# Kernel optimization log

Measured on AMD Instinct MI355X. Metric: run time of the kernel, lower is better.

## Reference

```python
import jax, jax.numpy as jnp
import numpy as np

N = 32768      # total nodes
E = 524288     # edges (avg degree 16)
HID = 256      # hidden_dim
H = 8          # heads
C = HID // H   # head dim = 32
G = 64         # graphs in batch
NPG = N // G   # nodes per graph = 512
EDIM = 2       # edge feature dim
NEG_SLOPE = 0.2  # PyG GATv2 default


def setup_inputs():
    key = jax.random.key(0)
    ks = jax.random.split(key, 12)
    s = 0.05
    return dict(
        x=jax.random.normal(ks[0], (N, HID), jnp.float32),
        edge_attr=jax.random.normal(ks[1], (E, EDIM), jnp.float32),
        # GATv2Conv params
        W_l=jax.random.normal(ks[2], (HID, HID), jnp.float32) * s,
        b_l=jnp.zeros((HID,), jnp.float32),
        W_r=jax.random.normal(ks[3], (HID, HID), jnp.float32) * s,
        b_r=jnp.zeros((HID,), jnp.float32),
        W_e=jax.random.normal(ks[4], (EDIM, HID), jnp.float32) * s,
        att=jax.random.normal(ks[5], (H, C), jnp.float32) * s,
        bias_gat=jnp.zeros((HID,), jnp.float32),
        # MultiheadAttention params (torch packed qkv layout)
        in_proj_w=jax.random.normal(ks[6], (3 * HID, HID), jnp.float32) * s,
        in_proj_b=jnp.zeros((3 * HID,), jnp.float32),
        out_proj_w=jax.random.normal(ks[7], (HID, HID), jnp.float32) * s,
        out_proj_b=jnp.zeros((HID,), jnp.float32),
        alpha_param=jnp.array(0.5, jnp.float32),
        # FFN
        W1=jax.random.normal(ks[8], (HID, 4 * HID), jnp.float32) * s,
        b1=jnp.zeros((4 * HID,), jnp.float32),
        W2=jax.random.normal(ks[9], (4 * HID, HID), jnp.float32) * s,
        b2=jnp.zeros((HID,), jnp.float32),
        # LayerNorms
        g1=jnp.ones((HID,), jnp.float32), be1=jnp.zeros((HID,), jnp.float32),
        g2=jnp.ones((HID,), jnp.float32), be2=jnp.zeros((HID,), jnp.float32),
        g3=jnp.ones((HID,), jnp.float32), be3=jnp.zeros((HID,), jnp.float32),
        edge_index=jax.random.randint(ks[10], (2, E), 0, N, jnp.int32),
        batch=jnp.repeat(jnp.arange(G, dtype=jnp.int32), NPG),
    )


def _ln(x, g, b, eps=1e-5):
    m = jnp.mean(x, -1, keepdims=True)
    v = jnp.mean((x - m) ** 2, -1, keepdims=True)
    return (x - m) * jax.lax.rsqrt(v + eps) * g + b


def _gatv2(x, edge_index, edge_attr, W_l, b_l, W_r, b_r, W_e, att, bias_gat):
    src, dst = edge_index[0], edge_index[1]
    # PyG add_self_loops with fill_value='mean': self-loop edge_attr at node i
    # is the mean of edge_attr over edges incoming to i (0 if none).
    deg = jax.ops.segment_sum(jnp.ones((E,), x.dtype), dst, num_segments=N)
    ea_mean = jax.ops.segment_sum(edge_attr, dst, num_segments=N) / jnp.maximum(deg, 1.0)[:, None]
    loop = jnp.arange(N, dtype=src.dtype)
    src2 = jnp.concatenate([src, loop])
    dst2 = jnp.concatenate([dst, loop])
    ea2 = jnp.concatenate([edge_attr, ea_mean], axis=0)  # [E+N, 2]
    xl = (x @ W_l + b_l).reshape(N, H, C)  # source transform (messages)
    xr = (x @ W_r + b_r).reshape(N, H, C)  # target transform
    ee = (ea2 @ W_e).reshape(-1, H, C)
    e = jax.nn.leaky_relu(xl[src2] + xr[dst2] + ee, NEG_SLOPE)  # [E+N, H, C]
    score = jnp.einsum('ehc,hc->eh', e, att)  # [E+N, H]
    # scatter softmax over incoming edges of each target node
    smax = jax.lax.stop_gradient(jax.ops.segment_max(score, dst2, num_segments=N))
    ex = jnp.exp(score - smax[dst2])
    ssum = jax.ops.segment_sum(ex, dst2, num_segments=N)
    alpha = ex / ssum[dst2]  # [E+N, H]
    out = jax.ops.segment_sum(alpha[:, :, None] * xl[src2], dst2, num_segments=N)
    return out.reshape(N, HID) + bias_gat


def _mha(xg, in_proj_w, in_proj_b, out_proj_w, out_proj_b):
    # xg: [G, NPG, HID]; torch nn.MultiheadAttention (batch_first, eval mode)
    qkv = xg @ in_proj_w.T + in_proj_b
    q, k, v = jnp.split(qkv, 3, axis=-1)
    q = q.reshape(G, NPG, H, C)
    k = k.reshape(G, NPG, H, C)
    v = v.reshape(G, NPG, H, C)
    scores = jnp.einsum('gqhd,gkhd->ghqk', q, k) / jnp.sqrt(jnp.float32(C))
    p = jax.nn.softmax(scores, axis=-1)
    o = jnp.einsum('ghqk,gkhd->gqhd', p, v).reshape(G, NPG, HID)
    return o @ out_proj_w.T + out_proj_b


def reference(x, edge_attr, W_l, b_l, W_r, b_r, W_e, att, bias_gat,
              in_proj_w, in_proj_b, out_proj_w, out_proj_b, alpha_param,
              W1, b1, W2, b2, g1, be1, g2, be2, g3, be3, edge_index, batch):
    local_out = _ln(
        _gatv2(x, edge_index, edge_attr, W_l, b_l, W_r, b_r, W_e, att, bias_gat),
        g1, be1)
    # batch is sorted with equal-sized graphs -> the per-graph ragged
    # attention loop equals one batched [G, NPG, NPG] attention
    xg = x.reshape(G, NPG, HID)
    global_out = _mha(xg, in_proj_w, in_proj_b, out_proj_w, out_proj_b).reshape(N, HID)
    global_out = _ln(global_out, g2, be2)
    a = jax.nn.sigmoid(alpha_param)
    combined = a * local_out + (1.0 - a) * global_out
    ffn = jax.nn.gelu(combined @ W1 + b1, approximate=False) @ W2 + b2
    return _ln(combined + ffn, g3, be3)
```

## Files before the change

kernel.cpp:

```cpp
#include <hip/hip_runtime.h>
#include <math.h>

#define N_NODES 32768
#define E_EDGES 524288
#define HIDDEN  256
#define NPG     512
#define NGRAPH  64
#define NHEAD   8
#define CDIM    32

typedef unsigned short bf16;
typedef __attribute__((ext_vector_type(8))) short short8;
typedef __attribute__((ext_vector_type(4))) float f4;

#define AS1 __attribute__((address_space(1)))
#define AS3 __attribute__((address_space(3)))

__device__ __forceinline__ void cp16(const bf16* g, bf16* l) {
    __builtin_amdgcn_global_load_lds((AS1 const unsigned int*)(const void*)g,
                                     (AS3 unsigned int*)(void*)l, 16, 0, 0);
}

__device__ inline float bf2f(unsigned short u) {
    union { unsigned int i; float f; } v; v.i = ((unsigned int)u) << 16; return v.f;
}
__device__ inline unsigned short f2bf(float f) {
    union { float f; unsigned int i; } v; v.f = f;
    unsigned int x = v.i;
    return (unsigned short)((x + 0x7FFFu + ((x >> 16) & 1u)) >> 16);
}
__device__ inline float4 load4(const float* p) { return *(const float4*)p; }
__device__ inline float4 load4(const bf16* p) {
    ushort4 u = *(const ushort4*)p;
    return make_float4(bf2f(u.x), bf2f(u.y), bf2f(u.z), bf2f(u.w));
}
__device__ inline void store4(float* p, float4 v) { *(float4*)p = v; }
__device__ inline void store4(bf16* p, float4 v) {
    ushort4 u; u.x = f2bf(v.x); u.y = f2bf(v.y); u.z = f2bf(v.z); u.w = f2bf(v.w);
    *(ushort4*)p = u;
}


__global__ void zero_kernel(float* deg, float* ea_sum, int* fill) {
    int i = blockIdx.x * blockDim.x + threadIdx.x;
    if (i < 2 * N_NODES) ea_sum[i] = 0.0f;
    if (i < N_NODES) { deg[i] = 0.0f; fill[i] = 0; }
}

__global__ void deg_kernel(const int* __restrict__ ei, const float* __restrict__ edge_attr,
                           float* deg, float* ea_sum) {
    int e = blockIdx.x * blockDim.x + threadIdx.x;
    if (e >= E_EDGES) return;
    int d = ei[E_EDGES + e];
    atomicAdd(&deg[d], 1.0f);
    atomicAdd(&ea_sum[2 * d + 0], edge_attr[2 * e + 0]);
    atomicAdd(&ea_sum[2 * d + 1], edge_attr[2 * e + 1]);
}

__global__ void eamean_kernel(const float* __restrict__ deg, float* ea_mean) {
    int i = blockIdx.x * blockDim.x + threadIdx.x;
    if (i >= N_NODES) return;
    float dm = fmaxf(deg[i], 1.0f);
    ea_mean[2 * i + 0] /= dm;
    ea_mean[2 * i + 1] /= dm;
}

__global__ __launch_bounds__(1024) void scan_kernel(const float* __restrict__ deg, int* row_ptr) {
    __shared__ int part[1024];
    int t = threadIdx.x;
    int base = t * 32;
    int loc[32];
    int s = 0;
    #pragma unroll
    for (int j = 0; j < 32; j++) {
        loc[j] = s;
        s += (int)deg[base + j] + 1;
    }
    int mysum = s;
    part[t] = s;
    __syncthreads();
    for (int off = 1; off < 1024; off <<= 1) {
        int v = 0;
        if (t >= off) v = part[t - off];
        __syncthreads();
        part[t] += v;
        __syncthreads();
    }
    int offset = part[t] - mysum;
    #pragma unroll
    for (int j = 0; j < 32; j++) row_ptr[base + j] = offset + loc[j];
    if (t == 1023) row_ptr[N_NODES] = part[1023];
}

__global__ void fill_kernel(const int* __restrict__ ei, const int* __restrict__ row_ptr,
                            int* fill, int* col) {
    int tid = blockIdx.x * blockDim.x + threadIdx.x;
    if (tid >= E_EDGES + N_NODES) return;
    int d;
    if (tid < E_EDGES) d = ei[E_EDGES + tid];
    else               d = tid - E_EDGES;
    int pos = row_ptr[d] + atomicAdd(&fill[d], 1);
    col[pos] = tid;
}

__global__ void convall(const float* __restrict__ x,
                        const float* __restrict__ W_l, const float* __restrict__ W_r,
                        const float* __restrict__ W1, const float* __restrict__ W2,
                        const float* __restrict__ in_proj_w, const float* __restrict__ out_proj_w,
                        const float* __restrict__ b_l, const float* __restrict__ b_r,
                        bf16* xb, bf16* wlrb, bf16* w1b, bf16* w2b,
                        bf16* wipb, bf16* wopb, float* blr)
{
    int b = blockIdx.x, t = threadIdx.x;
    if (b < 8192) {
        int i = b * 256 + t;
        store4(&xb[i * 4], *(const float4*)&x[i * 4]);
    } else if (b < 8448) {
        int i = (b - 8192) * 256 + t; int k = i >> 8, n = i & 255;
        wlrb[n * 256 + k] = f2bf(W_l[i]);
    } else if (b < 8704) {
        int i = (b - 8448) * 256 + t; int k = i >> 8, n = i & 255;
        wlrb[(256 + n) * 256 + k] = f2bf(W_r[i]);
    } else if (b < 9728) {
        int i = (b - 8704) * 256 + t; int k = i >> 10, n = i & 1023;
        w1b[n * 256 + k] = f2bf(W1[i]);
    } else if (b < 10752) {
        int i = (b - 9728) * 256 + t; int k = i >> 8, n = i & 255;
        w2b[n * 1024 + k] = f2bf(W2[i]);
    } else if (b < 10944) {
        int i = (b - 10752) * 256 + t;
        store4(&wipb[i * 4], *(const float4*)&in_proj_w[i * 4]);
    } else if (b < 11008) {
        int i = (b - 10944) * 256 + t;
        store4(&wopb[i * 4], *(const float4*)&out_proj_w[i * 4]);
    } else {
        blr[t] = b_l[t]; blr[256 + t] = b_r[t];
    }
}

template <int EPI>
__global__ __launch_bounds__(256) void mfma_gemm(
    const bf16* __restrict__ A, const bf16* __restrict__ Wb,
    const float* __restrict__ bias, const bf16* __restrict__ res,
    bf16* __restrict__ C, int M, int N, int K)
{
    __shared__ bf16 lds[2 * 128 * 64];
    bf16* As = lds;
    bf16* Bs = lds + 128 * 64;
    int tid = threadIdx.x;
    int wave = tid >> 6, lane = tid & 63;
    int quad = lane >> 4, l16 = lane & 15;
    int n0 = blockIdx.x * 128, m0 = blockIdx.y * 128;
    int wm = (wave & 1) * 64, wn = (wave >> 1) * 64;

    f4 acc[4][4] = {};

    int srow = tid >> 3;
    int scol = (tid & 7) * 8;

    for (int k0 = 0; k0 < K; k0 += 64) {
        #pragma unroll
        for (int i = 0; i < 4; i++) {
            int row = i * 32 + srow;
            cp16(&A[(size_t)(m0 + row) * K + k0 + scol], &As[row * 64 + scol]);
            cp16(&Wb[(size_t)(n0 + row) * K + k0 + scol], &Bs[row * 64 + scol]);
        }
        __syncthreads();
        #pragma unroll
        for (int ks = 0; ks < 2; ks++) {
            short8 af[4], bfr[4];
            #pragma unroll
            for (int mt = 0; mt < 4; mt++)
                af[mt] = *(const short8*)&As[(wm + mt * 16 + l16) * 64 + ks * 32 + quad * 8];
            #pragma unroll
            for (int nt = 0; nt < 4; nt++)
                bfr[nt] = *(const short8*)&Bs[(wn + nt * 16 + l16) * 64 + ks * 32 + quad * 8];
            #pragma unroll
            for (int mt = 0; mt < 4; mt++)
                #pragma unroll
                for (int nt = 0; nt < 4; nt++)
                    acc[mt][nt] = __builtin_amdgcn_mfma_f32_16x16x32_bf16(
                        af[mt], bfr[nt], acc[mt][nt], 0, 0, 0);
        }
        __syncthreads();
    }

    float* epi = (float*)lds + wave * 16 * 68;
    int row = lane >> 2;
    int cb = (lane & 3) * 16;
    int gn = n0 + wn + cb;
    float bb[16];
    *(float4*)&bb[0]  = *(const float4*)&bias[gn + 0];
    *(float4*)&bb[4]  = *(const float4*)&bias[gn + 4];
    *(float4*)&bb[8]  = *(const float4*)&bias[gn + 8];
    *(float4*)&bb[12] = *(const float4*)&bias[gn + 12];

    for (int mt = 0; mt < 4; mt++) {
        #pragma unroll
        for (int nt = 0; nt < 4; nt++)
            #pragma unroll
            for (int r = 0; r < 4; r++)
                epi[(quad * 4 + r) * 68 + nt * 16 + l16] = acc[mt][nt][r];
        float vv[16];
        *(float4*)&vv[0]  = *(float4*)&epi[row * 68 + cb + 0];
        *(float4*)&vv[4]  = *(float4*)&epi[row * 68 + cb + 4];
        *(float4*)&vv[8]  = *(float4*)&epi[row * 68 + cb + 8];
        *(float4*)&vv[12] = *(float4*)&epi[row * 68 + cb + 12];
        int gm = m0 + wm + mt * 16 + row;
        #pragma unroll
        for (int j = 0; j < 16; j++) vv[j] += bb[j];
        if (EPI == 1) {
            #pragma unroll
            for (int j = 0; j < 16; j++)
                vv[j] = 0.5f * vv[j] * (1.0f + erff(vv[j] * 0.70710678118654752f));
        } else if (EPI == 2) {
            ushort rr[16];
            const bf16* rp = &res[(size_t)gm * N + gn];
            *(int4*)&rr[0] = *(const int4*)&rp[0];
            *(int4*)&rr[8] = *(const int4*)&rp[8];
            #pragma unroll
            for (int j = 0; j < 16; j++) vv[j] += bf2f(rr[j]);
        }
        ushort o16[16];
        #pragma unroll
        for (int j = 0; j < 16; j++) o16[j] = f2bf(vv[j]);
        bf16* cp;
        if (EPI == 3) {
            bf16* dst = (gn < 256) ? C : (bf16*)res;
            int goff = (gn < 256) ? gn : gn - 256;
            cp = &dst[(size_t)gm * 256 + goff];
        } else {
            cp = &C[(size_t)gm * N + gn];
        }
        *(int4*)&cp[0] = *(int4*)&o16[0];
        *(int4*)&cp[8] = *(int4*)&o16[8];
    }
}

__global__ __launch_bounds__(256) void attn_mfma(
    const bf16* __restrict__ qkv, bf16* __restrict__ attnout)
{
    __shared__ bf16 Ks[128 * 40];
    __shared__ bf16 Vs[128 * 40];
    __shared__ bf16 Pb[4 * 64 * 40];
    __shared__ float lsumS[4][64];

    int b = blockIdx.x;
    int g = b >> 4, h = (b >> 1) & 7, hlf = b & 1;
    int tid = threadIdx.x;
    int wave = tid >> 6, lane = tid & 63;
    int quad = lane >> 4, l16 = lane & 15;
    int qbase = hlf * 256 + wave * 64;
    bf16* Pw = &Pb[wave * 64 * 40];
    const float SCALE = 0.17677669529663687f;

    short8 qf[4];
    #pragma unroll
    for (int qt = 0; qt < 4; qt++) {
        size_t node = (size_t)(g * NPG + qbase + qt * 16 + l16);
        qf[qt] = *(const short8*)&qkv[node * 768 + h * CDIM + quad * 8];
    }

    f4 oacc[4][2] = {};
    float ls[4] = {0.f, 0.f, 0.f, 0.f};

    for (int c = 0; c < 4; c++) {
        int kk0 = c * 128;
        __syncthreads();
        #pragma unroll
        for (int i = 0; i < 2; i++) {
            int idx = i * 256 + tid;
            int key = idx >> 2, kc = (idx & 3) * 8;
            const bf16* bp = &qkv[(size_t)(g * NPG + kk0 + key) * 768 + h * CDIM + kc];
            *(int4*)&Ks[key * 40 + kc] = *(const int4*)(bp + 256);
            *(int4*)&Vs[key * 40 + kc] = *(const int4*)(bp + 512);
        }
        __syncthreads();

        for (int sub = 0; sub < 4; sub++) {
            int ks0 = sub * 32;
            short8 kf[2];
            #pragma unroll
            for (int kt = 0; kt < 2; kt++)
                kf[kt] = *(const short8*)&Ks[(ks0 + kt * 16 + l16) * 40 + quad * 8];
            #pragma unroll
            for (int kt = 0; kt < 2; kt++) {
                #pragma unroll
                for (int qt = 0; qt < 4; qt++) {
                    f4 z = {0.f, 0.f, 0.f, 0.f};
                    f4 st = __builtin_amdgcn_mfma_f32_16x16x32_bf16(kf[kt], qf[qt], z, 0, 0, 0);
                    ushort pk[4];
                    float s4 = 0.f;
                    #pragma unroll
                    for (int r = 0; r < 4; r++) {
                        float p = __expf(st[r] * SCALE);
                        s4 += p;
                        pk[r] = f2bf(p);
                    }
                    ls[qt] += s4;
                    *(uint2*)&Pw[(qt * 16 + l16) * 40 + kt * 16 + quad * 4] = *(uint2*)pk;
                }
            }
            short8 vf[2];
            #pragma unroll
            for (int dt = 0; dt < 2; dt++) {
                ushort vtmp[8];
                #pragma unroll
                for (int j = 0; j < 8; j++)
                    vtmp[j] = Vs[(ks0 + quad * 8 + j) * 40 + dt * 16 + l16];
                vf[dt] = *(short8*)vtmp;
            }
            #pragma unroll
            for (int mt = 0; mt < 4; mt++) {
                short8 pf = *(const short8*)&Pw[(mt * 16 + l16) * 40 + quad * 8];
                #pragma unroll
                for (int dt = 0; dt < 2; dt++)
                    oacc[mt][dt] = __builtin_amdgcn_mfma_f32_16x16x32_bf16(
                        pf, vf[dt], oacc[mt][dt], 0, 0, 0);
            }
        }
    }

    #pragma unroll
    for (int qt = 0; qt < 4; qt++) {
        float l = ls[qt];
        l += __shfl_xor(l, 16);
        l += __shfl_xor(l, 32);
        if (quad == 0) lsumS[wave][qt * 16 + l16] = l;
    }
    __builtin_amdgcn_s_waitcnt(0);

    #pragma unroll
    for (int mt = 0; mt < 4; mt++) {
        #pragma unroll
        for (int dt = 0; dt < 2; dt++) {
            #pragma unroll
            for (int r = 0; r < 4; r++) {
                float denom = lsumS[wave][mt * 16 + quad * 4 + r];
                float v = oacc[mt][dt][r] / denom;
                size_t node = (size_t)(g * NPG + qbase + mt * 16 + quad * 4 + r);
                attnout[node * HIDDEN + h * CDIM + dt * 16 + l16] = f2bf(v);
            }
        }
    }
}

__device__ __forceinline__ void fetchmeta(
    int i, int re, int node, const int* __restrict__ col, const int* __restrict__ ei,
    const float* __restrict__ edge_attr, const float* __restrict__ ea_mean,
    int& s, float& a0, float& a1)
{
    if (i < re) {
        int e = col[i];
        if (e < E_EDGES) {
            s = ei[e]; a0 = edge_attr[2 * e]; a1 = edge_attr[2 * e + 1];
        } else {
            s = node; a0 = ea_mean[2 * node]; a1 = ea_mean[2 * node + 1];
        }
    } else {
        s = node; a0 = 0.f; a1 = 0.f;
    }
}

__global__ __launch_bounds__(256) void gat_kernel(
    const bf16* __restrict__ xl, const bf16* __restrict__ xr,
    const int* __restrict__ row_ptr, const int* __restrict__ col,
    const int* __restrict__ ei, const float* __restrict__ edge_attr,
    const float* __restrict__ ea_mean,
    const float* __restrict__ W_e, const float* __restrict__ att,
    const float* __restrict__ bias_gat,
    const float* __restrict__ g1, const float* __restrict__ be1,
    bf16* __restrict__ out)
{
    __shared__ float pacc[2][260];
    __shared__ float plsum[2][64];
    int wave = threadIdx.x >> 6;
    int lane = threadIdx.x & 63;
    int nloc = wave >> 1, half = wave & 1;
    int node = blockIdx.x * 2 + nloc;
    int cb = lane * 4;

    float4 xr4 = load4(&xr[(size_t)node * 256 + cb]);
    float4 we0 = *(const float4*)&W_e[cb];
    float4 we1 = *(const float4*)&W_e[HIDDEN + cb];
    float4 at4 = *(const float4*)&att[cb];

    int rs = row_ptr[node], re = row_ptr[node + 1];

    float lsum = 0.f;
    float acc0 = 0.f, acc1 = 0.f, acc2 = 0.f, acc3 = 0.f;

    int i0 = rs + half;
    int s0, s1; float a00, a01, a10, a11;
    fetchmeta(i0,     re, node, col, ei, edge_attr, ea_mean, s0, a00, a01);
    fetchmeta(i0 + 2, re, node, col, ei, edge_attr, ea_mean, s1, a10, a11);
    ushort4 xu0 = *(const ushort4*)&xl[(size_t)s0 * 256 + cb];

    for (int i = i0; i < re; i += 2) {
        int s2; float a20, a21;
        fetchmeta(i + 4, re, node, col, ei, edge_attr, ea_mean, s2, a20, a21);
        ushort4 xu1 = *(const ushort4*)&xl[(size_t)s1 * 256 + cb];

        float4 xl4 = make_float4(bf2f(xu0.x), bf2f(xu0.y), bf2f(xu0.z), bf2f(xu0.w));
        float t, p = 0.f;
        t = xl4.x + xr4.x + a00 * we0.x + a01 * we1.x; t = (t > 0.f) ? t : 0.2f * t; p += t * at4.x;
        t = xl4.y + xr4.y + a00 * we0.y + a01 * we1.y; t = (t > 0.f) ? t : 0.2f * t; p += t * at4.y;
        t = xl4.z + xr4.z + a00 * we0.z + a01 * we1.z; t = (t > 0.f) ? t : 0.2f * t; p += t * at4.z;
        t = xl4.w + xr4.w + a00 * we0.w + a01 * we1.w; t = (t > 0.f) ? t : 0.2f * t; p += t * at4.w;
        p += __shfl_xor(p, 1);
        p += __shfl_xor(p, 2);
        p += __shfl_xor(p, 4);
        float w = __expf(p);
        lsum += w;
        acc0 += w * xl4.x; acc1 += w * xl4.y; acc2 += w * xl4.z; acc3 += w * xl4.w;

        s0 = s1; a00 = a10; a01 = a11; xu0 = xu1;
        s1 = s2; a10 = a20; a11 = a21;
    }

    if (half) {
        plsum[nloc][lane] = lsum;
        pacc[nloc][cb + 0] = acc0; pacc[nloc][cb + 1] = acc1;
        pacc[nloc][cb + 2] = acc2; pacc[nloc][cb + 3] = acc3;
    }
    __syncthreads();
    if (!half) {
        lsum += plsum[nloc][lane];
        acc0 += pacc[nloc][cb + 0]; acc1 += pacc[nloc][cb + 1];
        acc2 += pacc[nloc][cb + 2]; acc3 += pacc[nloc][cb + 3];

        float inv = 1.0f / lsum;
        float v0 = acc0 * inv + bias_gat[cb + 0];
        float v1 = acc1 * inv + bias_gat[cb + 1];
        float v2 = acc2 * inv + bias_gat[cb + 2];
        float v3 = acc3 * inv + bias_gat[cb + 3];

        float s = v0 + v1 + v2 + v3;
        #pragma unroll
        for (int m = 1; m < 64; m <<= 1) s += __shfl_xor(s, m);
        float mean = s * (1.0f / 256.0f);
        float d0 = v0 - mean, d1 = v1 - mean, d2 = v2 - mean, d3 = v3 - mean;
        float sq = d0 * d0 + d1 * d1 + d2 * d2 + d3 * d3;
        #pragma unroll
        for (int m = 1; m < 64; m <<= 1) sq += __shfl_xor(sq, m);
        float rstd = rsqrtf(sq * (1.0f / 256.0f) + 1e-5f);
        float4 o;
        o.x = d0 * rstd * g1[cb + 0] + be1[cb + 0];
        o.y = d1 * rstd * g1[cb + 1] + be1[cb + 1];
        o.z = d2 * rstd * g1[cb + 2] + be1[cb + 2];
        o.w = d3 * rstd * g1[cb + 3] + be1[cb + 3];
        store4(&out[(size_t)node * HIDDEN + cb], o);
    }
}

__global__ __launch_bounds__(256) void combine_kernel(
    const bf16* __restrict__ gout, const bf16* __restrict__ localout,
    const float* __restrict__ alpha_p,
    const float* __restrict__ g2, const float* __restrict__ be2,
    bf16* __restrict__ combined)
{
    int wave = threadIdx.x >> 6;
    int lane = threadIdx.x & 63;
    int node = blockIdx.x * 4 + wave;
    int cb = lane * 4;
    float4 gv = load4(&gout[(size_t)node * HIDDEN + cb]);
    float s = gv.x + gv.y + gv.z + gv.w;
    #pragma unroll
    for (int m = 1; m < 64; m <<= 1) s += __shfl_xor(s, m);
    float mean = s * (1.0f / 256.0f);
    float d0 = gv.x - mean, d1 = gv.y - mean, d2 = gv.z - mean, d3 = gv.w - mean;
    float sq = d0 * d0 + d1 * d1 + d2 * d2 + d3 * d3;
    #pragma unroll
    for (int m = 1; m < 64; m <<= 1) sq += __shfl_xor(sq, m);
    float rstd = rsqrtf(sq * (1.0f / 256.0f) + 1e-5f);
    float n0 = d0 * rstd * g2[cb + 0] + be2[cb + 0];
    float n1 = d1 * rstd * g2[cb + 1] + be2[cb + 1];
    float n2 = d2 * rstd * g2[cb + 2] + be2[cb + 2];
    float n3 = d3 * rstd * g2[cb + 3] + be2[cb + 3];
    float a = 1.0f / (1.0f + __expf(-alpha_p[0]));
    float4 lv = load4(&localout[(size_t)node * HIDDEN + cb]);
    float4 o;
    o.x = a * lv.x + (1.0f - a) * n0;
    o.y = a * lv.y + (1.0f - a) * n1;
    o.z = a * lv.z + (1.0f - a) * n2;
    o.w = a * lv.w + (1.0f - a) * n3;
    store4(&combined[(size_t)node * HIDDEN + cb], o);
}

__global__ __launch_bounds__(256) void finalln_kernel(
    const bf16* __restrict__ ffn,
    const float* __restrict__ g3, const float* __restrict__ be3,
    float* __restrict__ out)
{
    int wave = threadIdx.x >> 6;
    int lane = threadIdx.x & 63;
    int node = blockIdx.x * 4 + wave;
    int cb = lane * 4;
    float4 v = load4(&ffn[(size_t)node * HIDDEN + cb]);
    float s = v.x + v.y + v.z + v.w;
    #pragma unroll
    for (int m = 1; m < 64; m <<= 1) s += __shfl_xor(s, m);
    float mean = s * (1.0f / 256.0f);
    float d0 = v.x - mean, d1 = v.y - mean, d2 = v.z - mean, d3 = v.w - mean;
    float sq = d0 * d0 + d1 * d1 + d2 * d2 + d3 * d3;
    #pragma unroll
    for (int m = 1; m < 64; m <<= 1) sq += __shfl_xor(sq, m);
    float rstd = rsqrtf(sq * (1.0f / 256.0f) + 1e-5f);
    float4 o;
    o.x = d0 * rstd * g3[cb + 0] + be3[cb + 0];
    o.y = d1 * rstd * g3[cb + 1] + be3[cb + 1];
    o.z = d2 * rstd * g3[cb + 2] + be3[cb + 2];
    o.w = d3 * rstd * g3[cb + 3] + be3[cb + 3];
    *(float4*)&out[(size_t)node * HIDDEN + cb] = o;
}

extern "C" void kernel_launch(void* const* d_in, const int* in_sizes, int n_in,
                              void* d_out, int out_size, void* d_ws, size_t ws_size,
                              hipStream_t stream) {
    const float* x          = (const float*)d_in[0];
    const float* edge_attr  = (const float*)d_in[1];
    const float* W_l        = (const float*)d_in[2];
    const float* b_l        = (const float*)d_in[3];
    const float* W_r        = (const float*)d_in[4];
    const float* b_r        = (const float*)d_in[5];
    const float* W_e        = (const float*)d_in[6];
    const float* att        = (const float*)d_in[7];
    const float* bias_gat   = (const float*)d_in[8];
    const float* in_proj_w  = (const float*)d_in[9];
    const float* in_proj_b  = (const float*)d_in[10];
    const float* out_proj_w = (const float*)d_in[11];
    const float* out_proj_b = (const float*)d_in[12];
    const float* alpha_p    = (const float*)d_in[13];
    const float* W1         = (const float*)d_in[14];
    const float* b1         = (const float*)d_in[15];
    const float* W2         = (const float*)d_in[16];
    const float* b2         = (const float*)d_in[17];
    const float* g1  = (const float*)d_in[18];
    const float* be1 = (const float*)d_in[19];
    const float* g2  = (const float*)d_in[20];
    const float* be2 = (const float*)d_in[21];
    const float* g3  = (const float*)d_in[22];
    const float* be3 = (const float*)d_in[23];
    const int* edge_index = (const int*)d_in[24];

    char* base = (char*)d_ws;
    const size_t MB = 1024 * 1024;
    const size_t KB = 1024;
    float* deg     = (float*)(base + 0);
    float* ea_mean = (float*)(base + 131072);
    int*   fill    = (int*)  (base + 393216);
    int*   row_ptr = (int*)  (base + 524288);
    int*   col     = (int*)  (base + 786432);
    bf16* wlrb = (bf16*)(base + 3 * MB);
    bf16* wipb = (bf16*)(base + 3 * MB + 256 * KB);
    bf16* wopb = (bf16*)(base + 3 * MB + 640 * KB);
    bf16* w1b  = (bf16*)(base + 3 * MB + 768 * KB);
    bf16* w2b  = (bf16*)(base + 3 * MB + 1280 * KB);
    float* blr = (float*)(base + 5 * MB);
    bf16* xb       = (bf16*)(base + 8 * MB);
    bf16* qkv      = (bf16*)(base + 24 * MB);
    bf16* attnout  = (bf16*)(base + 72 * MB);
    bf16* gout     = (bf16*)(base + 24 * MB);
    bf16* xl       = (bf16*)(base + 40 * MB);
    bf16* xr       = (bf16*)(base + 56 * MB);
    bf16* localout = (bf16*)(base + 72 * MB);
    bf16* combined = (bf16*)(base + 8 * MB);
    bf16* h1h      = (bf16*)(base + 24 * MB);
    bf16* ffn      = (bf16*)(base + 56 * MB);
    float* out = (float*)d_out;

    zero_kernel<<<(2 * N_NODES + 255) / 256, 256, 0, stream>>>(deg, ea_mean, fill);
    deg_kernel<<<E_EDGES / 256, 256, 0, stream>>>(edge_index, edge_attr, deg, ea_mean);
    eamean_kernel<<<N_NODES / 256, 256, 0, stream>>>(deg, ea_mean);
    scan_kernel<<<1, 1024, 0, stream>>>(deg, row_ptr);
    fill_kernel<<<(E_EDGES + N_NODES) / 256, 256, 0, stream>>>(edge_index, row_ptr, fill, col);

    convall<<<11009, 256, 0, stream>>>(x, W_l, W_r, W1, W2, in_proj_w, out_proj_w,
                                       b_l, b_r, xb, wlrb, w1b, w2b, wipb, wopb, blr);

    mfma_gemm<0><<<dim3(6, 256), 256, 0, stream>>>(
        xb, wipb, in_proj_b, (const bf16*)nullptr, qkv, N_NODES, 768, 256);
    attn_mfma<<<NGRAPH * NHEAD * 2, 256, 0, stream>>>(qkv, attnout);
    mfma_gemm<0><<<dim3(2, 256), 256, 0, stream>>>(
        attnout, wopb, out_proj_b, (const bf16*)nullptr, gout, N_NODES, 256, 256);

    mfma_gemm<3><<<dim3(4, 256), 256, 0, stream>>>(
        xb, wlrb, blr, (const bf16*)xr, xl, N_NODES, 512, 256);
    gat_kernel<<<N_NODES / 2, 256, 0, stream>>>(
        xl, xr, row_ptr, col, edge_index, edge_attr, ea_mean,
        W_e, att, bias_gat, g1, be1, localout);

    combine_kernel<<<N_NODES / 4, 256, 0, stream>>>(
        gout, localout, alpha_p, g2, be2, combined);

    for (int hh = 0; hh < 2; hh++) {
        const bf16* ch = combined + (size_t)hh * 16384 * 256;
        bf16* fh = ffn + (size_t)hh * 16384 * 256;
        mfma_gemm<1><<<dim3(8, 128), 256, 0, stream>>>(
            ch, w1b, b1, (const bf16*)nullptr, h1h, 16384, 1024, 256);
        mfma_gemm<2><<<dim3(2, 128), 256, 0, stream>>>(
            h1h, w2b, b2, ch, fh, 16384, 256, 1024);
    }

    finalln_kernel<<<N_NODES / 4, 256, 0, stream>>>(ffn, g3, be3, out);
}
```

Before: 616.3 us.

## Transpose V in LDS for attention and restructure GAT gather to one wave per node

The attention kernel now stores V transposed in shared memory, so each lane reads its MFMA B-operand as one 16-byte vector instead of eight strided scalar LDS reads. The GAT kernel drops the two-waves-per-node split and its LDS reduction. Each wave now handles one node and processes four edges per iteration, with four row gathers issued together and the next four edges' metadata prefetched. The gather change aims to raise memory-level parallelism and remove a block barrier, at the cost of more registers and wasted masked lanes on the tail of each edge list.

After: 664.7 us. +7.9%, slower.

```diff
diff --git a/kernel.cpp b/kernel.cpp
--- a/kernel.cpp
+++ b/kernel.cpp
@@ -241,7 +241,7 @@
     const bf16* __restrict__ qkv, bf16* __restrict__ attnout)
 {
     __shared__ bf16 Ks[128 * 40];
-    __shared__ bf16 Vs[128 * 40];
+    __shared__ bf16 Vt[32 * 136];
     __shared__ bf16 Pb[4 * 64 * 40];
     __shared__ float lsumS[4][64];
 
@@ -271,9 +271,17 @@
         for (int i = 0; i < 2; i++) {
             int idx = i * 256 + tid;
             int key = idx >> 2, kc = (idx & 3) * 8;
-            const bf16* bp = &qkv[(size_t)(g * NPG + kk0 + key) * 768 + h * CDIM + kc];
-            *(int4*)&Ks[key * 40 + kc] = *(const int4*)(bp + 256);
-            *(int4*)&Vs[key * 40 + kc] = *(const int4*)(bp + 512);
+            *(int4*)&Ks[key * 40 + kc] =
+                *(const int4*)&qkv[(size_t)(g * NPG + kk0 + key) * 768 + 256 + h * CDIM + kc];
+        }
+        {
+            int key = tid >> 1, dblk = (tid & 1) * 16;
+            ushort tmp[16];
+            const bf16* vp = &qkv[(size_t)(g * NPG + kk0 + key) * 768 + 512 + h * CDIM + dblk];
+            *(int4*)&tmp[0] = *(const int4*)&vp[0];
+            *(int4*)&tmp[8] = *(const int4*)&vp[8];
+            #pragma unroll
+            for (int j = 0; j < 16; j++) Vt[(dblk + j) * 136 + key] = tmp[j];
         }
         __syncthreads();
 
@@ -303,13 +311,8 @@
             }
             short8 vf[2];
             #pragma unroll
-            for (int dt = 0; dt < 2; dt++) {
-                ushort vtmp[8];
-                #pragma unroll
-                for (int j = 0; j < 8; j++)
-                    vtmp[j] = Vs[(ks0 + quad * 8 + j) * 40 + dt * 16 + l16];
-                vf[dt] = *(short8*)vtmp;
-            }
+            for (int dt = 0; dt < 2; dt++)
+                vf[dt] = *(const short8*)&Vt[(dt * 16 + l16) * 136 + ks0 + quad * 8];
             #pragma unroll
             for (int mt = 0; mt < 4; mt++) {
                 short8 pf = *(const short8*)&Pw[(mt * 16 + l16) * 40 + quad * 8];
@@ -342,23 +345,6 @@
                 attnout[node * HIDDEN + h * CDIM + dt * 16 + l16] = f2bf(v);
             }
         }
-    }
-}
-
-__device__ __forceinline__ void fetchmeta(
-    int i, int re, int node, const int* __restrict__ col, const int* __restrict__ ei,
-    const float* __restrict__ edge_attr, const float* __restrict__ ea_mean,
-    int& s, float& a0, float& a1)
-{
-    if (i < re) {
-        int e = col[i];
-        if (e < E_EDGES) {
-            s = ei[e]; a0 = edge_attr[2 * e]; a1 = edge_attr[2 * e + 1];
-        } else {
-            s = node; a0 = ea_mean[2 * node]; a1 = ea_mean[2 * node + 1];
-        }
-    } else {
-        s = node; a0 = 0.f; a1 = 0.f;
     }
 }
 
@@ -372,12 +358,9 @@
     const float* __restrict__ g1, const float* __restrict__ be1,
     bf16* __restrict__ out)
 {
-    __shared__ float pacc[2][260];
-    __shared__ float plsum[2][64];
     int wave = threadIdx.x >> 6;
     int lane = threadIdx.x & 63;
-    int nloc = wave >> 1, half = wave & 1;
-    int node = blockIdx.x * 2 + nloc;
+    int node = blockIdx.x * 4 + wave;
     int cb = lane * 4;
 
     float4 xr4 = load4(&xr[(size_t)node * 256 + cb]);
@@ -390,67 +373,75 @@
     float lsum = 0.f;
     float acc0 = 0.f, acc1 = 0.f, acc2 = 0.f, acc3 = 0.f;
 
-    int i0 = rs + half;
-    int s0, s1; float a00, a01, a10, a11;
-    fetchmeta(i0,     re, node, col, ei, edge_attr, ea_mean, s0, a00, a01);
-    fetchmeta(i0 + 2, re, node, col, ei, edge_attr, ea_mean, s1, a10, a11);
-    ushort4 xu0 = *(const ushort4*)&xl[(size_t)s0 * 256 + cb];
-
-    for (int i = i0; i < re; i += 2) {
-        int s2; float a20, a21;
-        fetchmeta(i + 4, re, node, col, ei, edge_attr, ea_mean, s2, a20, a21);
-        ushort4 xu1 = *(const ushort4*)&xl[(size_t)s1 * 256 + cb];
-
-        float4 xl4 = make_float4(bf2f(xu0.x), bf2f(xu0.y), bf2f(xu0.z), bf2f(xu0.w));
-        float t, p = 0.f;
-        t = xl4.x + xr4.x + a00 * we0.x + a01 * we1.x; t = (t > 0.f) ? t : 0.2f * t; p += t * at4.x;
-        t = xl4.y + xr4.y + a00 * we0.y + a01 * we1.y; t = (t > 0.f) ? t : 0.2f * t; p += t * at4.y;
-        t = xl4.z + xr4.z + a00 * we0.z + a01 * we1.z; t = (t > 0.f) ? t : 0.2f * t; p += t * at4.z;
-        t = xl4.w + xr4.w + a00 * we0.w + a01 * we1.w; t = (t > 0.f) ? t : 0.2f * t; p += t * at4.w;
-        p += __shfl_xor(p, 1);
-        p += __shfl_xor(p, 2);
-        p += __shfl_xor(p, 4);
-        float w = __expf(p);
-        lsum += w;
-        acc0 += w * xl4.x; acc1 += w * xl4.y; acc2 += w * xl4.z; acc3 += w * xl4.w;
-
-        s0 = s1; a00 = a10; a01 = a11; xu0 = xu1;
-        s1 = s2; a10 = a20; a11 = a21;
-    }
-
-    if (half) {
-        plsum[nloc][lane] = lsum;
-        pacc[nloc][cb + 0] = acc0; pacc[nloc][cb + 1] = acc1;
-        pacc[nloc][cb + 2] = acc2; pacc[nloc][cb + 3] = acc3;
-    }
-    __syncthreads();
-    if (!half) {
-        lsum += plsum[nloc][lane];
-        acc0 += pacc[nloc][cb + 0]; acc1 += pacc[nloc][cb + 1];
-        acc2 += pacc[nloc][cb + 2]; acc3 += pacc[nloc][cb + 3];
-
-        float inv = 1.0f / lsum;
-        float v0 = acc0 * inv + bias_gat[cb + 0];
-        float v1 = acc1 * inv + bias_gat[cb + 1];
-        float v2 = acc2 * inv + bias_gat[cb + 2];
-        float v3 = acc3 * inv + bias_gat[cb + 3];
-
-        float s = v0 + v1 + v2 + v3;
-        #pragma unroll
-        for (int m = 1; m < 64; m <<= 1) s += __shfl_xor(s, m);
-        float mean = s * (1.0f / 256.0f);
-        float d0 = v0 - mean, d1 = v1 - mean, d2 = v2 - mean, d3 = v3 - mean;
-        float sq = d0 * d0 + d1 * d1 + d2 * d2 + d3 * d3;
-        #pragma unroll
-        for (int m = 1; m < 64; m <<= 1) sq += __shfl_xor(sq, m);
-        float rstd = rsqrtf(sq * (1.0f / 256.0f) + 1e-5f);
-        float4 o;
-        o.x = d0 * rstd * g1[cb + 0] + be1[cb + 0];
-        o.y = d1 * rstd * g1[cb + 1] + be1[cb + 1];
-        o.z = d2 * rstd * g1[cb + 2] + be1[cb + 2];
-        o.w = d3 * rstd * g1[cb + 3] + be1[cb + 3];
-        store4(&out[(size_t)node * HIDDEN + cb], o);
-    }
+    int s[4]; float ax[4], ay[4];
+    #pragma unroll
+    for (int j = 0; j < 4; j++) {
+        int idx = rs + j;
+        if (idx < re) {
+            int e = col[idx];
+            if (e < E_EDGES) { s[j] = ei[e]; ax[j] = edge_attr[2 * e]; ay[j] = edge_attr[2 * e + 1]; }
+            else { s[j] = node; ax[j] = ea_mean[2 * node]; ay[j] = ea_mean[2 * node + 1]; }
+        } else { s[j] = node; ax[j] = 0.f; ay[j] = 0.f; }
+    }
+
+    for (int i = rs; i < re; i += 4) {
+        ushort4 xu[4];
+        #pragma unroll
+        for (int j = 0; j < 4; j++)
+            xu[j] = *(const ushort4*)&xl[(size_t)s[j] * 256 + cb];
+
+        int sn[4]; float axn[4], ayn[4];
+        int in0 = i + 4;
+        #pragma unroll
+        for (int j = 0; j < 4; j++) {
+            int idx = in0 + j;
+            if (idx < re) {
+                int e = col[idx];
+                if (e < E_EDGES) { sn[j] = ei[e]; axn[j] = edge_attr[2 * e]; ayn[j] = edge_attr[2 * e + 1]; }
+                else { sn[j] = node; axn[j] = ea_mean[2 * node]; ayn[j] = ea_mean[2 * node + 1]; }
+            } else { sn[j] = node; axn[j] = 0.f; ayn[j] = 0.f; }
+        }
+
+        #pragma unroll
+        for (int j = 0; j < 4; j++) {
+            float4 x4 = make_float4(bf2f(xu[j].x), bf2f(xu[j].y), bf2f(xu[j].z), bf2f(xu[j].w));
+            float t, p = 0.f;
+            t = x4.x + xr4.x + ax[j] * we0.x + ay[j] * we1.x; t = (t > 0.f) ? t : 0.2f * t; p += t * at4.x;
+            t = x4.y + xr4.y + ax[j] * we0.y + ay[j] * we1.y; t = (t > 0.f) ? t : 0.2f * t; p += t * at4.y;
+            t = x4.z + xr4.z + ax[j] * we0.z + ay[j] * we1.z; t = (t > 0.f) ? t : 0.2f * t; p += t * at4.z;
+            t = x4.w + xr4.w + ax[j] * we0.w + ay[j] * we1.w; t = (t > 0.f) ? t : 0.2f * t; p += t * at4.w;
+            p += __shfl_xor(p, 1);
+            p += __shfl_xor(p, 2);
+            p += __shfl_xor(p, 4);
+            float w = (i + j < re) ? __expf(p) : 0.f;
+            lsum += w;
+            acc0 += w * x4.x; acc1 += w * x4.y; acc2 += w * x4.z; acc3 += w * x4.w;
+        }
+        #pragma unroll
+        for (int j = 0; j < 4; j++) { s[j] = sn[j]; ax[j] = axn[j]; ay[j] = ayn[j]; }
+    }
+
+    float inv = 1.0f / lsum;
+    float v0 = acc0 * inv + bias_gat[cb + 0];
+    float v1 = acc1 * inv + bias_gat[cb + 1];
+    float v2 = acc2 * inv + bias_gat[cb + 2];
+    float v3 = acc3 * inv + bias_gat[cb + 3];
+
+    float sm = v0 + v1 + v2 + v3;
+    #pragma unroll
+    for (int m = 1; m < 64; m <<= 1) sm += __shfl_xor(sm, m);
+    float mean = sm * (1.0f / 256.0f);
+    float d0 = v0 - mean, d1 = v1 - mean, d2 = v2 - mean, d3 = v3 - mean;
+    float sq = d0 * d0 + d1 * d1 + d2 * d2 + d3 * d3;
+    #pragma unroll
+    for (int m = 1; m < 64; m <<= 1) sq += __shfl_xor(sq, m);
+    float rstd = rsqrtf(sq * (1.0f / 256.0f) + 1e-5f);
+    float4 o;
+    o.x = d0 * rstd * g1[cb + 0] + be1[cb + 0];
+    o.y = d1 * rstd * g1[cb + 1] + be1[cb + 1];
+    o.z = d2 * rstd * g1[cb + 2] + be1[cb + 2];
+    o.w = d3 * rstd * g1[cb + 3] + be1[cb + 3];
+    store4(&out[(size_t)node * HIDDEN + cb], o);
 }
 
 __global__ __launch_bounds__(256) void combine_kernel(
@@ -586,7 +577,7 @@
 
     mfma_gemm<3><<<dim3(4, 256), 256, 0, stream>>>(
         xb, wlrb, blr, (const bf16*)xr, xl, N_NODES, 512, 256);
-    gat_kernel<<<N_NODES / 2, 256, 0, stream>>>(
+    gat_kernel<<<N_NODES / 4, 256, 0, stream>>>(
         xl, xr, row_ptr, col, edge_index, edge_attr, ea_mean,
         W_e, att, bias_gat, g1, be1, localout);
 
```

## Fuse LayerNorm epilogues into out-proj and FFN2 GEMMs, split QKV outputs

Applied to the files above, without the earlier changes.

Adds a gemm_ln kernel that computes a full 256-wide output row tile per block and applies bias, residual, LayerNorm and the alpha blend (or the final LN to fp32) in the epilogue. This removes the separate combine and final-LN kernels and their round trips through global memory. The QKV projection now writes separate Q, K, V buffers through the slab-split epilogue. The attention kernel stores V transposed in LDS so it can be read as contiguous vectors instead of eight scalar gathers. The fused GEMM launches fewer blocks (512 or 256) with larger LDS use, which may reduce occupancy and parallelism, and the variance is computed as E[x²]−mean².

Measured after the change: 684.1 us. 11.0% more time.

```diff
diff --git a/kernel.cpp b/kernel.cpp
--- a/kernel.cpp
+++ b/kernel.cpp
@@ -108,33 +108,39 @@
                         const float* __restrict__ W1, const float* __restrict__ W2,
                         const float* __restrict__ in_proj_w, const float* __restrict__ out_proj_w,
                         const float* __restrict__ b_l, const float* __restrict__ b_r,
-                        bf16* xb, bf16* wlrb, bf16* w1b, bf16* w2b,
-                        bf16* wipb, bf16* wopb, float* blr)
+                        const float* __restrict__ in_proj_b,
+                        bf16* xb, bf16* wcat, bf16* w1b, bf16* w2b,
+                        bf16* wopb, float* bcat)
 {
     int b = blockIdx.x, t = threadIdx.x;
     if (b < 8192) {
         int i = b * 256 + t;
         store4(&xb[i * 4], *(const float4*)&x[i * 4]);
-    } else if (b < 8448) {
-        int i = (b - 8192) * 256 + t; int k = i >> 8, n = i & 255;
-        wlrb[n * 256 + k] = f2bf(W_l[i]);
-    } else if (b < 8704) {
-        int i = (b - 8448) * 256 + t; int k = i >> 8, n = i & 255;
-        wlrb[(256 + n) * 256 + k] = f2bf(W_r[i]);
-    } else if (b < 9728) {
-        int i = (b - 8704) * 256 + t; int k = i >> 10, n = i & 1023;
+    } else if (b < 8960) {
+        int i = (b - 8192) * 256 + t;
+        wcat[i] = f2bf(in_proj_w[i]);
+    } else if (b < 9216) {
+        int i = (b - 8960) * 256 + t; int k = i >> 8, n = i & 255;
+        wcat[(768 + n) * 256 + k] = f2bf(W_l[i]);
+    } else if (b < 9472) {
+        int i = (b - 9216) * 256 + t; int k = i >> 8, n = i & 255;
+        wcat[(1024 + n) * 256 + k] = f2bf(W_r[i]);
+    } else if (b < 10496) {
+        int i = (b - 9472) * 256 + t; int k = i >> 10, n = i & 1023;
         w1b[n * 256 + k] = f2bf(W1[i]);
-    } else if (b < 10752) {
-        int i = (b - 9728) * 256 + t; int k = i >> 8, n = i & 255;
+    } else if (b < 11520) {
+        int i = (b - 10496) * 256 + t; int k = i >> 8, n = i & 255;
         w2b[n * 1024 + k] = f2bf(W2[i]);
-    } else if (b < 10944) {
-        int i = (b - 10752) * 256 + t;
-        store4(&wipb[i * 4], *(const float4*)&in_proj_w[i * 4]);
-    } else if (b < 11008) {
-        int i = (b - 10944) * 256 + t;
+    } else if (b < 11584) {
+        int i = (b - 11520) * 256 + t;
         store4(&wopb[i * 4], *(const float4*)&out_proj_w[i * 4]);
     } else {
-        blr[t] = b_l[t]; blr[256 + t] = b_r[t];
+        #pragma unroll
+        for (int j = 0; j < 5; j++) {
+            int idx = j * 256 + t;
+            bcat[idx] = (idx < 768) ? in_proj_b[idx]
+                      : (idx < 1024) ? b_l[idx - 768] : b_r[idx - 1024];
+        }
     }
 }
 
@@ -142,7 +148,7 @@
 __global__ __launch_bounds__(256) void mfma_gemm(
     const bf16* __restrict__ A, const bf16* __restrict__ Wb,
     const float* __restrict__ bias, const bf16* __restrict__ res,
-    bf16* __restrict__ C, int M, int N, int K)
+    bf16* __restrict__ C, int M, int N, int K, bf16* __restrict__ d2)
 {
     __shared__ bf16 lds[2 * 128 * 64];
     bf16* As = lds;
@@ -154,7 +160,6 @@
     int wm = (wave & 1) * 64, wn = (wave >> 1) * 64;
 
     f4 acc[4][4] = {};
-
     int srow = tid >> 3;
     int scol = (tid & 7) * 8;
 
@@ -213,22 +218,15 @@
             #pragma unroll
             for (int j = 0; j < 16; j++)
                 vv[j] = 0.5f * vv[j] * (1.0f + erff(vv[j] * 0.70710678118654752f));
-        } else if (EPI == 2) {
-            ushort rr[16];
-            const bf16* rp = &res[(size_t)gm * N + gn];
-            *(int4*)&rr[0] = *(const int4*)&rp[0];
-            *(int4*)&rr[8] = *(const int4*)&rp[8];
-            #pragma unroll
-            for (int j = 0; j < 16; j++) vv[j] += bf2f(rr[j]);
         }
         ushort o16[16];
         #pragma unroll
         for (int j = 0; j < 16; j++) o16[j] = f2bf(vv[j]);
         bf16* cp;
         if (EPI == 3) {
-            bf16* dst = (gn < 256) ? C : (bf16*)res;
-            int goff = (gn < 256) ? gn : gn - 256;
-            cp = &dst[(size_t)gm * 256 + goff];
+            int slab = gn >> 8;
+            bf16* dst = (slab == 0) ? C : (slab == 1) ? (bf16*)res : d2;
+            cp = &dst[(size_t)gm * 256 + (gn & 255)];
         } else {
             cp = &C[(size_t)gm * N + gn];
         }
@@ -237,11 +235,134 @@
     }
 }
 
+template <int FINAL>
+__global__ __launch_bounds__(256) void gemm_ln(
+    const bf16* __restrict__ A, const bf16* __restrict__ Wb,
+    const float* __restrict__ bias, const bf16* __restrict__ aux,
+    const float* __restrict__ alpha_p,
+    const float* __restrict__ gamma, const float* __restrict__ beta,
+    void* Cout, int M, int K)
+{
+    __shared__ bf16 As[64 * 64];
+    __shared__ bf16 Bs[256 * 64];
+    __shared__ float rsum[4][64];
+    __shared__ float rsq[4][64];
+    int tid = threadIdx.x;
+    int wave = tid >> 6, lane = tid & 63;
+    int quad = lane >> 4, l16 = lane & 15;
+    int m0 = blockIdx.x * 64;
+    int wn = wave * 64;
+    f4 acc[4][4] = {};
+    int srow = tid >> 3, scol = (tid & 7) * 8;
+
+    for (int k0 = 0; k0 < K; k0 += 64) {
+        #pragma unroll
+        for (int i = 0; i < 10; i++) {
+            int vr = i * 32 + srow;
+            if (vr < 64)
+                cp16(&A[(size_t)(m0 + vr) * K + k0 + scol], &As[vr * 64 + scol]);
+            else
+                cp16(&Wb[(size_t)(vr - 64) * K + k0 + scol], &Bs[(vr - 64) * 64 + scol]);
+        }
+        __syncthreads();
+        #pragma unroll
+        for (int ks = 0; ks < 2; ks++) {
+            short8 af[4], bfr[4];
+            #pragma unroll
+            for (int mt = 0; mt < 4; mt++)
+                af[mt] = *(const short8*)&As[(mt * 16 + l16) * 64 + ks * 32 + quad * 8];
+            #pragma unroll
+            for (int nt = 0; nt < 4; nt++)
+                bfr[nt] = *(const short8*)&Bs[(wn + nt * 16 + l16) * 64 + ks * 32 + quad * 8];
+            #pragma unroll
+            for (int mt = 0; mt < 4; mt++)
+                #pragma unroll
+                for (int nt = 0; nt < 4; nt++)
+                    acc[mt][nt] = __builtin_amdgcn_mfma_f32_16x16x32_bf16(
+                        af[mt], bfr[nt], acc[mt][nt], 0, 0, 0);
+        }
+        __syncthreads();
+    }
+
+    float bb[4];
+    #pragma unroll
+    for (int nt = 0; nt < 4; nt++) bb[nt] = bias[wn + nt * 16 + l16];
+    #pragma unroll
+    for (int mt = 0; mt < 4; mt++)
+        #pragma unroll
+        for (int nt = 0; nt < 4; nt++)
+            #pragma unroll
+            for (int r = 0; r < 4; r++) {
+                acc[mt][nt][r] += bb[nt];
+                if (FINAL) {
+                    int row = mt * 16 + quad * 4 + r;
+                    int col = wn + nt * 16 + l16;
+                    acc[mt][nt][r] += bf2f(aux[(size_t)(m0 + row) * 256 + col]);
+                }
+            }
+
+    #pragma unroll
+    for (int mt = 0; mt < 4; mt++)
+        #pragma unroll
+        for (int r = 0; r < 4; r++) {
+            float s = 0.f, qq = 0.f;
+            #pragma unroll
+            for (int nt = 0; nt < 4; nt++) {
+                float v = acc[mt][nt][r];
+                s += v; qq += v * v;
+            }
+            s += __shfl_xor(s, 1); qq += __shfl_xor(qq, 1);
+            s += __shfl_xor(s, 2); qq += __shfl_xor(qq, 2);
+            s += __shfl_xor(s, 4); qq += __shfl_xor(qq, 4);
+            s += __shfl_xor(s, 8); qq += __shfl_xor(qq, 8);
+            if (l16 == 0) {
+                int row = mt * 16 + quad * 4 + r;
+                rsum[wave][row] = s;
+                rsq[wave][row] = qq;
+            }
+        }
+    __syncthreads();
+
+    float aco = 0.f;
+    if (!FINAL) aco = 1.f / (1.f + __expf(-alpha_p[0]));
+    float gg[4], bt[4];
+    #pragma unroll
+    for (int nt = 0; nt < 4; nt++) {
+        gg[nt] = gamma[wn + nt * 16 + l16];
+        bt[nt] = beta[wn + nt * 16 + l16];
+    }
+
+    #pragma unroll
+    for (int mt = 0; mt < 4; mt++)
+        #pragma unroll
+        for (int r = 0; r < 4; r++) {
+            int row = mt * 16 + quad * 4 + r;
+            float tot  = rsum[0][row] + rsum[1][row] + rsum[2][row] + rsum[3][row];
+            float totq = rsq[0][row] + rsq[1][row] + rsq[2][row] + rsq[3][row];
+            float mean = tot * (1.0f / 256.0f);
+            float var = totq * (1.0f / 256.0f) - mean * mean;
+            float rstd = rsqrtf(var + 1e-5f);
+            size_t gm = (size_t)(m0 + row);
+            #pragma unroll
+            for (int nt = 0; nt < 4; nt++) {
+                int col = wn + nt * 16 + l16;
+                float nv = (acc[mt][nt][r] - mean) * rstd * gg[nt] + bt[nt];
+                if (FINAL) {
+                    ((float*)Cout)[gm * 256 + col] = nv;
+                } else {
+                    float lv = bf2f(aux[gm * 256 + col]);
+                    ((bf16*)Cout)[gm * 256 + col] = f2bf(aco * lv + (1.f - aco) * nv);
+                }
+            }
+        }
+}
+
 __global__ __launch_bounds__(256) void attn_mfma(
-    const bf16* __restrict__ qkv, bf16* __restrict__ attnout)
+    const bf16* __restrict__ q, const bf16* __restrict__ k, const bf16* __restrict__ v,
+    bf16* __restrict__ attnout)
 {
     __shared__ bf16 Ks[128 * 40];
-    __shared__ bf16 Vs[128 * 40];
+    __shared__ bf16 Vt[32 * 136];
     __shared__ bf16 Pb[4 * 64 * 40];
     __shared__ float lsumS[4][64];
 
@@ -258,7 +379,7 @@
     #pragma unroll
     for (int qt = 0; qt < 4; qt++) {
         size_t node = (size_t)(g * NPG + qbase + qt * 16 + l16);
-        qf[qt] = *(const short8*)&qkv[node * 768 + h * CDIM + quad * 8];
+        qf[qt] = *(const short8*)&q[node * 256 + h * CDIM + quad * 8];
     }
 
     f4 oacc[4][2] = {};
@@ -271,9 +392,17 @@
         for (int i = 0; i < 2; i++) {
             int idx = i * 256 + tid;
             int key = idx >> 2, kc = (idx & 3) * 8;
-            const bf16* bp = &qkv[(size_t)(g * NPG + kk0 + key) * 768 + h * CDIM + kc];
-            *(int4*)&Ks[key * 40 + kc] = *(const int4*)(bp + 256);
-            *(int4*)&Vs[key * 40 + kc] = *(const int4*)(bp + 512);
+            *(int4*)&Ks[key * 40 + kc] =
+                *(const int4*)&k[(size_t)(g * NPG + kk0 + key) * 256 + h * CDIM + kc];
+        }
+        {
+            int key = tid >> 1, dblk = (tid & 1) * 16;
+            ushort tmp[16];
+            const bf16* vp = &v[(size_t)(g * NPG + kk0 + key) * 256 + h * CDIM + dblk];
+            *(int4*)&tmp[0] = *(const int4*)&vp[0];
+            *(int4*)&tmp[8] = *(const int4*)&vp[8];
+            #pragma unroll
+            for (int j = 0; j < 16; j++) Vt[(dblk + j) * 136 + key] = tmp[j];
         }
         __syncthreads();
 
@@ -303,13 +432,8 @@
             }
             short8 vf[2];
             #pragma unroll
-            for (int dt = 0; dt < 2; dt++) {
-                ushort vtmp[8];
-                #pragma unroll
-                for (int j = 0; j < 8; j++)
-                    vtmp[j] = Vs[(ks0 + quad * 8 + j) * 40 + dt * 16 + l16];
-                vf[dt] = *(short8*)vtmp;
-            }
+            for (int dt = 0; dt < 2; dt++)
+                vf[dt] = *(const short8*)&Vt[(dt * 16 + l16) * 136 + ks0 + quad * 8];
             #pragma unroll
             for (int mt = 0; mt < 4; mt++) {
                 short8 pf = *(const short8*)&Pw[(mt * 16 + l16) * 40 + quad * 8];
@@ -337,9 +461,9 @@
             #pragma unroll
             for (int r = 0; r < 4; r++) {
                 float denom = lsumS[wave][mt * 16 + quad * 4 + r];
-                float v = oacc[mt][dt][r] / denom;
+                float val = oacc[mt][dt][r] / denom;
                 size_t node = (size_t)(g * NPG + qbase + mt * 16 + quad * 4 + r);
-                attnout[node * HIDDEN + h * CDIM + dt * 16 + l16] = f2bf(v);
+                attnout[node * 256 + h * CDIM + dt * 16 + l16] = f2bf(val);
             }
         }
     }
@@ -451,67 +575,6 @@
         o.w = d3 * rstd * g1[cb + 3] + be1[cb + 3];
         store4(&out[(size_t)node * HIDDEN + cb], o);
     }
-}
-
-__global__ __launch_bounds__(256) void combine_kernel(
-    const bf16* __restrict__ gout, const bf16* __restrict__ localout,
-    const float* __restrict__ alpha_p,
-    const float* __restrict__ g2, const float* __restrict__ be2,
-    bf16* __restrict__ combined)
-{
-    int wave = threadIdx.x >> 6;
-    int lane = threadIdx.x & 63;
-    int node = blockIdx.x * 4 + wave;
-    int cb = lane * 4;
-    float4 gv = load4(&gout[(size_t)node * HIDDEN + cb]);
-    float s = gv.x + gv.y + gv.z + gv.w;
-    #pragma unroll
-    for (int m = 1; m < 64; m <<= 1) s += __shfl_xor(s, m);
-    float mean = s * (1.0f / 256.0f);
-    float d0 = gv.x - mean, d1 = gv.y - mean, d2 = gv.z - mean, d3 = gv.w - mean;
-    float sq = d0 * d0 + d1 * d1 + d2 * d2 + d3 * d3;
-    #pragma unroll
-    for (int m = 1; m < 64; m <<= 1) sq += __shfl_xor(sq, m);
-    float rstd = rsqrtf(sq * (1.0f / 256.0f) + 1e-5f);
-    float n0 = d0 * rstd * g2[cb + 0] + be2[cb + 0];
-    float n1 = d1 * rstd * g2[cb + 1] + be2[cb + 1];
-    float n2 = d2 * rstd * g2[cb + 2] + be2[cb + 2];
-    float n3 = d3 * rstd * g2[cb + 3] + be2[cb + 3];
-    float a = 1.0f / (1.0f + __expf(-alpha_p[0]));
-    float4 lv = load4(&localout[(size_t)node * HIDDEN + cb]);
-    float4 o;
-    o.x = a * lv.x + (1.0f - a) * n0;
-    o.y = a * lv.y + (1.0f - a) * n1;
-    o.z = a * lv.z + (1.0f - a) * n2;
-    o.w = a * lv.w + (1.0f - a) * n3;
-    store4(&combined[(size_t)node * HIDDEN + cb], o);
-}
-
-__global__ __launch_bounds__(256) void finalln_kernel(
-    const bf16* __restrict__ ffn,
-    const float* __restrict__ g3, const float* __restrict__ be3,
-    float* __restrict__ out)
-{
-    int wave = threadIdx.x >> 6;
-    int lane = threadIdx.x & 63;
-    int node = blockIdx.x * 4 + wave;
-    int cb = lane * 4;
-    float4 v = load4(&ffn[(size_t)node * HIDDEN + cb]);
-    float s = v.x + v.y + v.z + v.w;
-    #pragma unroll
-    for (int m = 1; m < 64; m <<= 1) s += __shfl_xor(s, m);
-    float mean = s * (1.0f / 256.0f);
-    float d0 = v.x - mean, d1 = v.y - mean, d2 = v.z - mean, d3 = v.w - mean;
-    float sq = d0 * d0 + d1 * d1 + d2 * d2 + d3 * d3;
-    #pragma unroll
-    for (int m = 1; m < 64; m <<= 1) sq += __shfl_xor(sq, m);
-    float rstd = rsqrtf(sq * (1.0f / 256.0f) + 1e-5f);
-    float4 o;
-    o.x = d0 * rstd * g3[cb + 0] + be3[cb + 0];
-    o.y = d1 * rstd * g3[cb + 1] + be3[cb + 1];
-    o.z = d2 * rstd * g3[cb + 2] + be3[cb + 2];
-    o.w = d3 * rstd * g3[cb + 3] + be3[cb + 3];
-    *(float4*)&out[(size_t)node * HIDDEN + cb] = o;
 }
 
 extern "C" void kernel_launch(void* const* d_in, const int* in_sizes, int n_in,
@@ -551,22 +614,21 @@
     int*   fill    = (int*)  (base + 393216);
     int*   row_ptr = (int*)  (base + 524288);
     int*   col     = (int*)  (base + 786432);
-    bf16* wlrb = (bf16*)(base + 3 * MB);
-    bf16* wipb = (bf16*)(base + 3 * MB + 256 * KB);
-    bf16* wopb = (bf16*)(base + 3 * MB + 640 * KB);
-    bf16* w1b  = (bf16*)(base + 3 * MB + 768 * KB);
-    bf16* w2b  = (bf16*)(base + 3 * MB + 1280 * KB);
-    float* blr = (float*)(base + 5 * MB);
-    bf16* xb       = (bf16*)(base + 8 * MB);
-    bf16* qkv      = (bf16*)(base + 24 * MB);
-    bf16* attnout  = (bf16*)(base + 72 * MB);
-    bf16* gout     = (bf16*)(base + 24 * MB);
-    bf16* xl       = (bf16*)(base + 40 * MB);
-    bf16* xr       = (bf16*)(base + 56 * MB);
-    bf16* localout = (bf16*)(base + 72 * MB);
-    bf16* combined = (bf16*)(base + 8 * MB);
-    bf16* h1h      = (bf16*)(base + 24 * MB);
-    bf16* ffn      = (bf16*)(base + 56 * MB);
+    bf16* wcat = (bf16*)(base + 3 * MB);
+    bf16* w1b  = (bf16*)(base + 3 * MB + 704 * KB);
+    bf16* w2b  = (bf16*)(base + 3 * MB + 1216 * KB);
+    bf16* wopb = (bf16*)(base + 3 * MB + 1728 * KB);
+    float* bcat = (float*)(base + 5 * MB);
+    bf16* xb       = (bf16*)(base + 6 * MB);
+    bf16* xl       = (bf16*)(base + 22 * MB);
+    bf16* xr       = (bf16*)(base + 38 * MB);
+    bf16* localout = (bf16*)(base + 54 * MB);
+    bf16* qb       = (bf16*)(base + 22 * MB);
+    bf16* kb       = (bf16*)(base + 38 * MB);
+    bf16* vb       = (bf16*)(base + 70 * MB);
+    bf16* attnout  = (bf16*)(base + 6 * MB);
+    bf16* combined = (bf16*)(base + 22 * MB);
+    bf16* h1h      = (bf16*)(base + 38 * MB);
     float* out = (float*)d_out;
 
     zero_kernel<<<(2 * N_NODES + 255) / 256, 256, 0, stream>>>(deg, ea_mean, fill);
@@ -575,32 +637,28 @@
     scan_kernel<<<1, 1024, 0, stream>>>(deg, row_ptr);
     fill_kernel<<<(E_EDGES + N_NODES) / 256, 256, 0, stream>>>(edge_index, row_ptr, fill, col);
 
-    convall<<<11009, 256, 0, stream>>>(x, W_l, W_r, W1, W2, in_proj_w, out_proj_w,
-                                       b_l, b_r, xb, wlrb, w1b, w2b, wipb, wopb, blr);
-
-    mfma_gemm<0><<<dim3(6, 256), 256, 0, stream>>>(
-        xb, wipb, in_proj_b, (const bf16*)nullptr, qkv, N_NODES, 768, 256);
-    attn_mfma<<<NGRAPH * NHEAD * 2, 256, 0, stream>>>(qkv, attnout);
-    mfma_gemm<0><<<dim3(2, 256), 256, 0, stream>>>(
-        attnout, wopb, out_proj_b, (const bf16*)nullptr, gout, N_NODES, 256, 256);
+    convall<<<11585, 256, 0, stream>>>(x, W_l, W_r, W1, W2, in_proj_w, out_proj_w,
+                                       b_l, b_r, in_proj_b, xb, wcat, w1b, w2b, wopb, bcat);
 
     mfma_gemm<3><<<dim3(4, 256), 256, 0, stream>>>(
-        xb, wlrb, blr, (const bf16*)xr, xl, N_NODES, 512, 256);
+        xb, wcat + 768 * 256, bcat + 768, xr, xl, N_NODES, 512, 256, (bf16*)nullptr);
     gat_kernel<<<N_NODES / 2, 256, 0, stream>>>(
         xl, xr, row_ptr, col, edge_index, edge_attr, ea_mean,
         W_e, att, bias_gat, g1, be1, localout);
 
-    combine_kernel<<<N_NODES / 4, 256, 0, stream>>>(
-        gout, localout, alpha_p, g2, be2, combined);
+    mfma_gemm<3><<<dim3(6, 256), 256, 0, stream>>>(
+        xb, wcat, bcat, kb, qb, N_NODES, 768, 256, vb);
+    attn_mfma<<<NGRAPH * NHEAD * 2, 256, 0, stream>>>(qb, kb, vb, attnout);
+    gemm_ln<0><<<512, 256, 0, stream>>>(
+        attnout, wopb, out_proj_b, localout, alpha_p, g2, be2,
+        (void*)combined, N_NODES, 256);
 
     for (int hh = 0; hh < 2; hh++) {
         const bf16* ch = combined + (size_t)hh * 16384 * 256;
-        bf16* fh = ffn + (size_t)hh * 16384 * 256;
+        float* oh = out + (size_t)hh * 16384 * 256;
         mfma_gemm<1><<<dim3(8, 128), 256, 0, stream>>>(
-            ch, w1b, b1, (const bf16*)nullptr, h1h, 16384, 1024, 256);
-        mfma_gemm<2><<<dim3(2, 128), 256, 0, stream>>>(
-            h1h, w2b, b2, ch, fh, 16384, 256, 1024);
-    }
-
-    finalln_kernel<<<N_NODES / 4, 256, 0, stream>>>(ffn, g3, be3, out);
-}
+            ch, w1b, b1, (const bf16*)nullptr, h1h, 16384, 1024, 256, (bf16*)nullptr);
+        gemm_ln<1><<<256, 256, 0, stream>>>(
+            h1h, w2b, b2, ch, alpha_p, g3, be3, (void*)oh, 16384, 1024);
+    }
+}
```
